# Optimization experiments

Hardware: AMD Instinct MI355X
Metric: run time of the kernel (lower is better)

Reference implementation:

```python
import jax, jax.numpy as jnp
import numpy as np

D, S, L, W, H, V = 64, 64, 64, 300, 300, 50000
NEG = jnp.float32(-9999999.0)


def setup_inputs() -> dict:
    key = jax.random.key(0)
    ks = jax.random.split(key, 16)
    n = lambda k, shape, s=0.05: jax.random.normal(k, shape, dtype=jnp.float32) * s
    return {
        "word_indices": jax.random.randint(ks[0], (D, S, L), 0, V),
        "E": n(ks[1], (V, W), 0.1),
        "W_sent": n(ks[2], (H, W)), "b_sent": jnp.zeros((H,), jnp.float32),
        "W_par": n(ks[3], (H, H)), "b_par": jnp.zeros((H,), jnp.float32),
        "W_ch": n(ks[4], (H, H)), "b_ch": jnp.zeros((H,), jnp.float32),
        "w_root": n(ks[5], (H,)), "b_root": jnp.zeros((), jnp.float32),
        "root_embed": n(ks[6], (H,)),
        "W_r": n(ks[7], (H, 3 * H)), "b_r": jnp.zeros((H,), jnp.float32),
        "W_cls": n(ks[8], (2, H)), "b_cls": jnp.zeros((2,), jnp.float32),
    }


def reference(word_indices, E, W_sent, b_sent, W_par, b_par, W_ch, b_ch,
              w_root, b_root, root_embed, W_r, b_r, W_cls, b_cls):
    lrelu = lambda x: jax.nn.leaky_relu(x, 0.01)
    # Ragged pad+gather stage of the original, dense here (all lengths == L)
    word_embed = E[word_indices]                 # [D,S,L,W]
    # 0.5*(X[l-1] + reverse(reverse(X))[l-1]) == X[l-1]; LSTM outputs unused in source
    x_last = word_embed[:, :, -1, :]             # [D,S,W]
    enc = lrelu(x_last @ W_sent.T + b_sent)      # [D,S,H] sentence encodings
    # Pairwise parent-child edge scores (O(S^2) dots in the original loops)
    P = lrelu(enc @ W_par.T + b_par)             # [D,S,H]
    C = lrelu(enc @ W_ch.T + b_ch)               # [D,S,H]
    A = jnp.einsum('dih,djh->dij', P, C)         # [D,S,S]
    A = jnp.where(jnp.eye(S, dtype=bool)[None], NEG, A)
    A = jax.nn.softmax(A, axis=1)                # Softmax(dim=0) per doc: over parents i
    scores = enc @ w_root + b_root               # [D,S] root scores
    fri = jax.nn.softmax(scores, axis=1)         # Softmax(dim=0) over sentences
    # ri[i] = r_embeds([enc_i, sum_k A[k,i]*enc_k + fri_i*root, enc_i*sum_k A[i,k]])
    tmp = jnp.einsum('dki,dkh->dih', A, enc)     # [D,S,H]
    agg = tmp + fri[..., None] * root_embed      # [D,S,H]
    tmp3 = enc * A.sum(axis=2, keepdims=True)    # [D,S,H]
    ri = lrelu(jnp.concatenate([enc, agg, tmp3], axis=-1) @ W_r.T + b_r)  # [D,S,H]
    final = ri.mean(axis=1)                      # [D,H]
    out = final @ W_cls.T + b_cls                # [D,2]
    return out, A, fri
```

## Files before the change

### kernel.cpp

```cpp
#include <hip/hip_runtime.h>

#define NEG_INF (-9999999.0f)

typedef __attribute__((ext_vector_type(8))) short bf16x8;
typedef __attribute__((ext_vector_type(4))) float f32x4;
typedef unsigned short us;
typedef unsigned int u32;

#define MFMA16 __builtin_amdgcn_mfma_f32_16x16x32_bf16

__device__ __forceinline__ float b2f(us u) {
  union { unsigned int i; float f; } x; x.i = ((unsigned int)u) << 16; return x.f;
}
__device__ __forceinline__ us f2b(float f) {
  union { float f; unsigned int i; } x; x.f = f;
  unsigned int r = x.i + 0x7fffu + ((x.i >> 16) & 1u);
  return (us)(r >> 16);
}
__device__ __forceinline__ float lrelu(float v) { return v > 0.f ? v : 0.01f * v; }
__device__ __forceinline__ bf16x8 ld8(const us* p) { return *reinterpret_cast<const bf16x8*>(p); }
__device__ __forceinline__ int swz(int row) { return (row & 7) << 4; }

__global__ __launch_bounds__(256) void k_prep0(
    const float* __restrict__ Ws, us* __restrict__ Wsb) {
  int gid = blockIdx.x * 256 + threadIdx.x;
  for (int i = gid; i < 320 * 320; i += 128 * 256) {
    int r = i / 320, c = i - r * 320;
    Wsb[i] = (r < 300 && c < 300) ? f2b(Ws[r * 300 + c]) : (us)0;
  }
}

template<int M, int NT, int KS>
__device__ __forceinline__ void sweepM(const us* __restrict__ Alds, const int (&rr)[M],
    int q, int lo, const us* __restrict__ Bg, int n0, f32x4 (&acc)[M][NT]) {
  const char* ab = (const char*)Alds;
  int ao[M], sw[M];
#pragma unroll
  for (int m = 0; m < M; ++m) { ao[m] = rr[m] * 640; sw[m] = swz(rr[m]); }
  const us* br[NT];
#pragma unroll
  for (int t = 0; t < NT; ++t)
    br[t] = Bg + (long)((n0 + t) * 16 + lo) * 320 + 8 * q;
  bf16x8 aC[M], aN[M], b0[NT], b1[NT];
#pragma unroll
  for (int m = 0; m < M; ++m) {
    aC[m] = *(const bf16x8*)(ab + ao[m] + ((16 * q) ^ sw[m]));
    aN[m] = *(const bf16x8*)(ab + ao[m] + ((64 + 16 * q) ^ sw[m]));
  }
#pragma unroll
  for (int t = 0; t < NT; ++t) b0[t] = ld8(br[t]);
#pragma unroll
  for (int t = 0; t < NT; ++t) b1[t] = ld8(br[t] + 32);
#pragma unroll
  for (int ks = 0; ks < KS - 2; ++ks) {
    bf16x8 aF[M], bF[NT];
    const int kb = 64 * (ks + 2) + 16 * q;
#pragma unroll
    for (int m = 0; m < M; ++m) aF[m] = *(const bf16x8*)(ab + ao[m] + (kb ^ sw[m]));
#pragma unroll
    for (int t = 0; t < NT; ++t) bF[t] = ld8(br[t] + (ks + 2) * 32);
#pragma unroll
    for (int t = 0; t < NT; ++t)
#pragma unroll
      for (int m = 0; m < M; ++m)
        acc[m][t] = MFMA16(aC[m], b0[t], acc[m][t], 0, 0, 0);
#pragma unroll
    for (int m = 0; m < M; ++m) { aC[m] = aN[m]; aN[m] = aF[m]; }
#pragma unroll
    for (int t = 0; t < NT; ++t) { b0[t] = b1[t]; b1[t] = bF[t]; }
  }
#pragma unroll
  for (int t = 0; t < NT; ++t)
#pragma unroll
    for (int m = 0; m < M; ++m) acc[m][t] = MFMA16(aC[m], b0[t], acc[m][t], 0, 0, 0);
#pragma unroll
  for (int t = 0; t < NT; ++t)
#pragma unroll
    for (int m = 0; m < M; ++m) acc[m][t] = MFMA16(aN[m], b1[t], acc[m][t], 0, 0, 0);
}

template<int NT, int KS>
__device__ __forceinline__ void sweepT2(const us* __restrict__ es, int q, int lo,
    const us* __restrict__ Ag, int n0, f32x4 (&acc)[2][NT]) {
  const char* eb = (const char*)es;
  int bo[2] = { lo * 640, (lo + 16) * 640 };
  int sb[2] = { swz(lo), swz(lo + 16) };
  const us* ar[NT];
#pragma unroll
  for (int t = 0; t < NT; ++t)
    ar[t] = Ag + (long)((n0 + t) * 16 + lo) * 320 + 8 * q;
  bf16x8 a0[NT], a1[NT], bC[2], bN[2];
#pragma unroll
  for (int t = 0; t < NT; ++t) a0[t] = ld8(ar[t]);
#pragma unroll
  for (int h = 0; h < 2; ++h)
    bC[h] = *(const bf16x8*)(eb + bo[h] + ((16 * q) ^ sb[h]));
#pragma unroll
  for (int t = 0; t < NT; ++t) a1[t] = ld8(ar[t] + 32);
#pragma unroll
  for (int h = 0; h < 2; ++h)
    bN[h] = *(const bf16x8*)(eb + bo[h] + ((64 + 16 * q) ^ sb[h]));
#pragma unroll
  for (int ks = 0; ks < KS - 2; ++ks) {
    bf16x8 a2[NT], bF[2];
    const int kb = 64 * (ks + 2) + 16 * q;
#pragma unroll
    for (int t = 0; t < NT; ++t) a2[t] = ld8(ar[t] + (ks + 2) * 32);
#pragma unroll
    for (int h = 0; h < 2; ++h)
      bF[h] = *(const bf16x8*)(eb + bo[h] + (kb ^ sb[h]));
#pragma unroll
    for (int t = 0; t < NT; ++t) {
      acc[0][t] = MFMA16(a0[t], bC[0], acc[0][t], 0, 0, 0);
      acc[1][t] = MFMA16(a0[t], bC[1], acc[1][t], 0, 0, 0);
    }
#pragma unroll
    for (int t = 0; t < NT; ++t) { a0[t] = a1[t]; a1[t] = a2[t]; }
#pragma unroll
    for (int h = 0; h < 2; ++h) { bC[h] = bN[h]; bN[h] = bF[h]; }
  }
#pragma unroll
  for (int t = 0; t < NT; ++t) {
    acc[0][t] = MFMA16(a0[t], bC[0], acc[0][t], 0, 0, 0);
    acc[1][t] = MFMA16(a0[t], bC[1], acc[1][t], 0, 0, 0);
  }
#pragma unroll
  for (int t = 0; t < NT; ++t) {
    acc[0][t] = MFMA16(a1[t], bN[0], acc[0][t], 0, 0, 0);
    acc[1][t] = MFMA16(a1[t], bN[1], acc[1][t], 0, 0, 0);
  }
}

template<int NT>
__device__ __forceinline__ void sweepG(const us* __restrict__ Ab,
    const us* __restrict__ Bb, int m0, int nt0, int lo, int q, int ksn, f32x4* acc) {
  const us* ar = Ab + (long)(m0 + lo) * 320 + 8 * q;
  const us* br[NT];
#pragma unroll
  for (int t = 0; t < NT; ++t)
    br[t] = Bb + (long)((nt0 + t) * 16 + lo) * 320 + 8 * q;
  bf16x8 a0 = ld8(ar), a1 = ld8(ar + 32);
  bf16x8 b0[NT], b1[NT];
#pragma unroll
  for (int t = 0; t < NT; ++t) b0[t] = ld8(br[t]);
#pragma unroll
  for (int t = 0; t < NT; ++t) b1[t] = ld8(br[t] + 32);
  for (int ks = 0; ks < ksn - 2; ++ks) {
    bf16x8 a2 = ld8(ar + (ks + 2) * 32);
    bf16x8 b2[NT];
#pragma unroll
    for (int t = 0; t < NT; ++t) b2[t] = ld8(br[t] + (ks + 2) * 32);
#pragma unroll
    for (int t = 0; t < NT; ++t)
      acc[t] = MFMA16(a0, b0[t], acc[t], 0, 0, 0);
    a0 = a1; a1 = a2;
#pragma unroll
    for (int t = 0; t < NT; ++t) { b0[t] = b1[t]; b1[t] = b2[t]; }
  }
#pragma unroll
  for (int t = 0; t < NT; ++t)
    acc[t] = MFMA16(a0, b0[t], acc[t], 0, 0, 0);
#pragma unroll
  for (int t = 0; t < NT; ++t)
    acc[t] = MFMA16(a1, b1[t], acc[t], 0, 0, 0);
}

__global__ __launch_bounds__(256) void k_encprep(
    const int* __restrict__ wi, const float* __restrict__ E,
    const us* __restrict__ Wsb, const float* __restrict__ b_sent,
    const float* __restrict__ w_root,
    const float* __restrict__ Wp, const float* __restrict__ Wc,
    const float* __restrict__ Wr, const float* __restrict__ root,
    us* __restrict__ encG, float* __restrict__ scG,
    us* __restrict__ Wpb, us* __restrict__ Wcb, us* __restrict__ Wr3b,
    float* __restrict__ c2) {
  int t = threadIdx.x;
  if (blockIdx.y == 1) {
    int gid = blockIdx.x * 256 + t;
    const int stride = 256 * 256;
    for (int i = gid; i < 5 * 102400; i += stride) {
      int p = i / 102400, rem = i - p * 102400;
      int r = rem / 320, c = rem - r * 320;
      us v = 0;
      if (r < 300 && c < 300) {
        if (p == 0)      v = f2b(Wp[r * 300 + c]);
        else if (p == 1) v = f2b(Wc[r * 300 + c]);
        else             v = f2b(Wr[r * 900 + (p - 2) * 300 + c]);
      }
      if (p == 0)      Wpb[rem] = v;
      else if (p == 1) Wcb[rem] = v;
      else             Wr3b[(p - 2) * 102400 + rem] = v;
    }
    if (gid < 2560) {
      int c = gid >> 3, p = gid & 7;
      float s = 0.f;
      if (c < 300)
        for (int h = p; h < 300; h += 8) s = fmaf(Wr[c * 900 + 300 + h], root[h], s);
      s += __shfl_xor(s, 1); s += __shfl_xor(s, 2); s += __shfl_xor(s, 4);
      if (p == 0) c2[c] = s;
    }
    return;
  }
  __shared__ __align__(16) us xs[16 * 320];
  __shared__ __align__(16) us es[16 * 320];
  int r0g = blockIdx.x * 16;
  {
    int row = t >> 4, p = t & 15;
    int widx = wi[((r0g + row) << 6) + 63];
    const float4* er = (const float4*)(E + (long)widx * 300);
    char* rowb = (char*)xs + row * 640;
    int sw = swz(row);
    for (int j = p; j < 75; j += 16) {
      float4 v = er[j];
      *(ushort4*)(rowb + ((8 * j) ^ sw)) =
          make_ushort4(f2b(v.x), f2b(v.y), f2b(v.z), f2b(v.w));
    }
    for (int c = 300 + p; c < 320; c += 16)
      *(us*)(rowb + ((2 * c) ^ sw)) = 0;
  }
  __syncthreads();
  int w = t >> 6, lane = t & 63, lo = lane & 15, q = lane >> 4;
  const f32x4 z4 = {0.f, 0.f, 0.f, 0.f};
  int rr[1] = { lo };
  f32x4 acc[1][5];
#pragma unroll
  for (int b = 0; b < 5; ++b) acc[0][b] = z4;
  sweepM<1, 5, 10>(xs, rr, q, lo, Wsb, w * 5, acc);
#pragma unroll
  for (int tt = 0; tt < 5; ++tt) {
    int col = (w * 5 + tt) * 16 + lo;
    float bb = (col < 300) ? b_sent[col] : 0.f;
#pragma unroll
    for (int r = 0; r < 4; ++r) {
      int row = 4 * q + r;
      us hv = (col < 300) ? f2b(lrelu(acc[0][tt][r] + bb)) : (us)0;
      *(us*)((char*)es + row * 640 + ((2 * col) ^ swz(row))) = hv;
      encG[(long)(r0g + row) * 320 + col] = hv;
    }
  }
  __syncthreads();
  {
    int row = t >> 4, p = t & 15;
    float s = 0.f;
    for (int cch = p; cch < 38; cch += 16) {
      bf16x8 v = *(const bf16x8*)((const char*)es + row * 640 + ((16 * cch) ^ swz(row)));
#pragma unroll
      for (int e = 0; e < 8; ++e) {
        int h = cch * 8 + e;
        if (h < 300) s = fmaf(b2f((us)v[e]), w_root[h], s);
      }
    }
    s += __shfl_xor(s, 1); s += __shfl_xor(s, 2); s += __shfl_xor(s, 4); s += __shfl_xor(s, 8);
    if (p == 0) scG[r0g + row] = s;
  }
}

__global__ __launch_bounds__(256) void k_panels(
    const us* __restrict__ encG,
    const us* __restrict__ Wpb, const us* __restrict__ Wcb, const us* __restrict__ Wrb,
    const float* __restrict__ b_par, const float* __restrict__ b_ch,
    us* __restrict__ Pg, us* __restrict__ Cg, us* __restrict__ G1g, us* __restrict__ G3g,
    us* __restrict__ G2eT) {
  __shared__ __align__(16) us es[32 * 320];
  int t = threadIdx.x, task = blockIdx.y, rt = blockIdx.x;
  {
    const float4* src = (const float4*)(encG + (long)rt * 32 * 320);
    for (int i = t; i < 1280; i += 256) {
      int row = i / 40, c16 = i - row * 40;
      float4 v = src[i];
      *(float4*)((char*)es + row * 640 + ((c16 * 16) ^ swz(row))) = v;
    }
  }
  __syncthreads();
  int w = t >> 6, lane = t & 63, lo = lane & 15, q = lane >> 4;
  const f32x4 z4 = {0.f, 0.f, 0.f, 0.f};
  if (task == 4) {
    f32x4 acc[2][5];
#pragma unroll
    for (int a = 0; a < 2; ++a)
#pragma unroll
      for (int b = 0; b < 5; ++b) acc[a][b] = z4;
    sweepT2<5, 10>(es, q, lo, Wrb + 102400, w * 5, acc);
#pragma unroll
    for (int half = 0; half < 2; ++half)
#pragma unroll
      for (int tt = 0; tt < 5; ++tt)
#pragma unroll
        for (int r = 0; r < 4; ++r) {
          int h = (w * 5 + tt) * 16 + 4 * q + r;
          G2eT[(long)h * 4096 + rt * 32 + half * 16 + lo] =
              (h < 300) ? f2b(acc[half][tt][r]) : (us)0;
        }
  } else {
    const us* Bg = (task == 0) ? Wpb : (task == 1) ? Wcb : (task == 2) ? Wrb : Wrb + 204800;
    int rr[2] = { lo, 16 + lo };
    f32x4 acc[2][5];
#pragma unroll
    for (int a = 0; a < 2; ++a)
#pragma unroll
      for (int b = 0; b < 5; ++b) acc[a][b] = z4;
    sweepM<2, 5, 10>(es, rr, q, lo, Bg, w * 5, acc);
    if (task < 2) {
      const float* bias = (task == 0) ? b_par : b_ch;
      us* outb = (task == 0) ? Pg : Cg;
#pragma unroll
      for (int m = 0; m < 2; ++m)
#pragma unroll
        for (int tt = 0; tt < 5; ++tt) {
          int col = (w * 5 + tt) * 16 + lo;
          float bb = (col < 300) ? bias[col] : 0.f;
#pragma unroll
          for (int r = 0; r < 4; ++r) {
            int row = rt * 32 + m * 16 + 4 * q + r;
            outb[(long)row * 320 + col] =
                (col < 300) ? f2b(lrelu(acc[m][tt][r] + bb)) : (us)0;
          }
        }
    } else {
      us* outb = (task == 2) ? G1g : G3g;
#pragma unroll
      for (int m = 0; m < 2; ++m)
#pragma unroll
        for (int tt = 0; tt < 5; ++tt) {
          int col = (w * 5 + tt) * 16 + lo;
          if (col < 300)
#pragma unroll
            for (int r = 0; r < 4; ++r)
              outb[(long)(rt * 32 + m * 16 + 4 * q + r) * 320 + col] = f2b(acc[m][tt][r]);
        }
    }
  }
}

__global__ __launch_bounds__(512) void k_doc(
    const us* __restrict__ Pg, const us* __restrict__ Cg, const us* __restrict__ G2eT,
    const us* __restrict__ G1g, const us* __restrict__ G3g,
    const float* __restrict__ scG, const float* __restrict__ c2,
    const float* __restrict__ b_r, const float* __restrict__ W_cls,
    const float* __restrict__ b_cls,
    float* __restrict__ outp, float* __restrict__ outA, float* __restrict__ outF) {
  __shared__ __align__(16) float LA[64 * 68];
  __shared__ __align__(16) us AtL[64 * 72];
  __shared__ float pm[512], ps[512];
  __shared__ float friS[64], rsS[64];
  __shared__ float finP2[4 * 320];
  int d = blockIdx.x, t = threadIdx.x;
  int w = t >> 6, lane = t & 63, lo = lane & 15, q = lane >> 4;
  const f32x4 z4 = {0.f, 0.f, 0.f, 0.f};

  if (t < 64) {
    float sc = scG[d * 64 + t], m = sc;
#pragma unroll
    for (int o = 32; o > 0; o >>= 1) m = fmaxf(m, __shfl_xor(m, o));
    float e = expf(sc - m), sum = e;
#pragma unroll
    for (int o = 32; o > 0; o >>= 1) sum += __shfl_xor(sum, o);
    float f = e / sum;
    friS[t] = f;
    outF[d * 64 + t] = f;
  }

  {
    const us* Pd = Pg + (long)d * 64 * 320;
    const us* Cd = Cg + (long)d * 64 * 320;
    int m = w >> 1, np = (w & 1) * 2;
    f32x4 acc2[2] = { z4, z4 };
    sweepG<2>(Pd, Cd, m * 16, np, lo, q, 10, acc2);
#pragma unroll
    for (int r = 0; r < 4; ++r) {
      int row = m * 16 + 4 * q + r;
      int c0 = np * 16 + lo, c1 = c0 + 16;
      LA[row * 68 + c0] = (row == c0) ? NEG_INF : acc2[0][r];
      LA[row * 68 + c1] = (row == c1) ? NEG_INF : acc2[1][r];
    }
  }
  __syncthreads();

  {
    int j = lane;
    float mx = -3.0e38f;
#pragma unroll
    for (int ii = 0; ii < 8; ++ii) mx = fmaxf(mx, LA[(w * 8 + ii) * 68 + j]);
    pm[w * 64 + j] = mx;
    __syncthreads();
    float gm = pm[j];
#pragma unroll
    for (int k = 1; k < 8; ++k) gm = fmaxf(gm, pm[k * 64 + j]);
    float ev[8], ss = 0.f;
#pragma unroll
    for (int ii = 0; ii < 8; ++ii) {
      float e = expf(LA[(w * 8 + ii) * 68 + j] - gm);
      ev[ii] = e; ss += e;
    }
    ps[w * 64 + j] = ss;
    __syncthreads();
    float tot = ps[j];
#pragma unroll
    for (int k = 1; k < 8; ++k) tot += ps[k * 64 + j];
    float inv = 1.f / tot;
    float* Ad = outA + (long)d * 4096;
#pragma unroll
    for (int ii = 0; ii < 8; ++ii) {
      int i = w * 8 + ii;
      float a = ev[ii] * inv;
      Ad[i * 64 + j] = a;
      AtL[j * 72 + i] = f2b(a);
      LA[i * 68 + j] = a;
    }
  }
  __syncthreads();
  if (t < 64) {
    float s = 0.f;
    for (int jj = 0; jj < 64; ++jj) s += LA[t * 68 + jj];
    rsS[t] = s;
  }
  __syncthreads();

  {
    int mg = w & 3, nh = w >> 2;
    f32x4 a10[10];
#pragma unroll
    for (int b = 0; b < 10; ++b) a10[b] = z4;
#pragma unroll
    for (int ks = 0; ks < 2; ++ks) {
      bf16x8 aA = ld8(AtL + (mg * 16 + lo) * 72 + 32 * ks + 8 * q);
#pragma unroll
      for (int tt = 0; tt < 10; ++tt) {
        bf16x8 bv = ld8(G2eT + (long)((nh * 10 + tt) * 16 + lo) * 4096 +
                        d * 64 + 32 * ks + 8 * q);
        a10[tt] = MFMA16(aA, bv, a10[tt], 0, 0, 0);
      }
    }
#pragma unroll
    for (int tt = 0; tt < 10; ++tt) {
      int col = (nh * 10 + tt) * 16 + lo;
      if (col < 300) {
        float bb = b_r[col], cc = c2[col];
        float csum = 0.f;
#pragma unroll
        for (int r = 0; r < 4; ++r) {
          int i = mg * 16 + 4 * q + r;
          float g1 = b2f(G1g[(long)(d * 64 + i) * 320 + col]);
          float g3 = b2f(G3g[(long)(d * 64 + i) * 320 + col]);
          csum += lrelu(a10[tt][r] + g1 + rsS[i] * g3 + friS[i] * cc + bb);
        }
        csum += __shfl_xor(csum, 16);
        csum += __shfl_xor(csum, 32);
        if (q == 0) finP2[mg * 320 + col] = csum;
      }
    }
  }
  __syncthreads();

  if (t < 128) {
    int cls = t >> 6, ln = t & 63;
    float s = 0.f;
    for (int h = ln; h < 300; h += 64)
      s += (finP2[h] + finP2[320 + h] + finP2[640 + h] + finP2[960 + h]) *
           W_cls[cls * 300 + h];
#pragma unroll
    for (int o = 32; o > 0; o >>= 1) s += __shfl_xor(s, o);
    if (ln == 0) outp[d * 2 + cls] = s * 0.015625f + b_cls[cls];
  }
}

extern "C" void kernel_launch(void* const* d_in, const int* in_sizes, int n_in,
                              void* d_out, int out_size, void* d_ws, size_t ws_size,
                              hipStream_t stream) {
  const int*   wi     = (const int*)d_in[0];
  const float* E      = (const float*)d_in[1];
  const float* W_sent = (const float*)d_in[2];
  const float* b_sent = (const float*)d_in[3];
  const float* W_par  = (const float*)d_in[4];
  const float* b_par  = (const float*)d_in[5];
  const float* W_ch   = (const float*)d_in[6];
  const float* b_ch   = (const float*)d_in[7];
  const float* w_root = (const float*)d_in[8];
  const float* b_root = (const float*)d_in[9];  (void)b_root;
  const float* root_e = (const float*)d_in[10];
  const float* W_r    = (const float*)d_in[11];
  const float* b_r    = (const float*)d_in[12];
  const float* W_cls  = (const float*)d_in[13];
  const float* b_cls  = (const float*)d_in[14];

  us* B = (us*)d_ws;
  us* Wsb   = B;
  us* Wpb   = B + 102400;
  us* Wcb   = B + 204800;
  us* Wr3b  = B + 307200;
  float* c2 = (float*)(B + 614400);
  us* encG  = B + 615040;
  us* Pg    = B + 1925760;
  us* Cg    = B + 3236480;
  us* G1g   = B + 4547200;
  us* G3g   = B + 5857920;
  us* G2eT  = B + 7168640;
  float* scG = (float*)(B + 8479360);

  float* outp = (float*)d_out;
  float* outA = outp + 128;
  float* outF = outp + 128 + 262144;

  k_prep0<<<128, 256, 0, stream>>>(W_sent, Wsb);
  k_encprep<<<dim3(256, 2), 256, 0, stream>>>(wi, E, Wsb, b_sent, w_root,
                                              W_par, W_ch, W_r, root_e,
                                              encG, scG, Wpb, Wcb, Wr3b, c2);
  k_panels<<<dim3(128, 5), 256, 0, stream>>>(encG, Wpb, Wcb, Wr3b,
                                             b_par, b_ch, Pg, Cg, G1g, G3g, G2eT);
  k_doc<<<64, 512, 0, stream>>>(Pg, Cg, G2eT, G1g, G3g, scG, c2,
                                b_r, W_cls, b_cls, outp, outA, outF);
}
```

Baseline: 174.1 us.

## Enlarge row tiles and store G1/G3 transposed for coalesced per-document reads

k_encprep now encodes 32 rows per block instead of 16, and its weight-conversion work moves from a second grid dimension into extra x-blocks (288 blocks in total). k_panels processes 64 rows per block, and a generalized sweepT computes G1 and G3 in transposed layout alongside G2eT. k_doc can then load four consecutive G1/G3 values per lane as one vector instead of strided scalar loads. The aim is more weight reuse per block and better-coalesced reads in the doc kernel, at the cost of fewer blocks (lower parallelism) and higher register pressure.

```diff
diff --git a/kernel.cpp b/kernel.cpp
--- a/kernel.cpp
+++ b/kernel.cpp
@@ -79,56 +79,55 @@
     for (int m = 0; m < M; ++m) acc[m][t] = MFMA16(aN[m], b1[t], acc[m][t], 0, 0, 0);
 }
 
-template<int NT, int KS>
-__device__ __forceinline__ void sweepT2(const us* __restrict__ es, int q, int lo,
-    const us* __restrict__ Ag, int n0, f32x4 (&acc)[2][NT]) {
+template<int NB, int NT, int KS>
+__device__ __forceinline__ void sweepT(const us* __restrict__ es, int q, int lo,
+    const us* __restrict__ Ag, int n0, f32x4 (&acc)[NB][NT]) {
   const char* eb = (const char*)es;
-  int bo[2] = { lo * 640, (lo + 16) * 640 };
-  int sb[2] = { swz(lo), swz(lo + 16) };
+  int bo[NB], sb[NB];
+#pragma unroll
+  for (int h = 0; h < NB; ++h) { bo[h] = (lo + 16 * h) * 640; sb[h] = swz(lo + 16 * h); }
   const us* ar[NT];
 #pragma unroll
   for (int t = 0; t < NT; ++t)
     ar[t] = Ag + (long)((n0 + t) * 16 + lo) * 320 + 8 * q;
-  bf16x8 a0[NT], a1[NT], bC[2], bN[2];
+  bf16x8 a0[NT], a1[NT], bC[NB], bN[NB];
 #pragma unroll
   for (int t = 0; t < NT; ++t) a0[t] = ld8(ar[t]);
 #pragma unroll
-  for (int h = 0; h < 2; ++h)
+  for (int h = 0; h < NB; ++h)
     bC[h] = *(const bf16x8*)(eb + bo[h] + ((16 * q) ^ sb[h]));
 #pragma unroll
   for (int t = 0; t < NT; ++t) a1[t] = ld8(ar[t] + 32);
 #pragma unroll
-  for (int h = 0; h < 2; ++h)
+  for (int h = 0; h < NB; ++h)
     bN[h] = *(const bf16x8*)(eb + bo[h] + ((64 + 16 * q) ^ sb[h]));
 #pragma unroll
   for (int ks = 0; ks < KS - 2; ++ks) {
-    bf16x8 a2[NT], bF[2];
+    bf16x8 a2[NT], bF[NB];
     const int kb = 64 * (ks + 2) + 16 * q;
 #pragma unroll
     for (int t = 0; t < NT; ++t) a2[t] = ld8(ar[t] + (ks + 2) * 32);
 #pragma unroll
-    for (int h = 0; h < 2; ++h)
+    for (int h = 0; h < NB; ++h)
       bF[h] = *(const bf16x8*)(eb + bo[h] + (kb ^ sb[h]));
 #pragma unroll
-    for (int t = 0; t < NT; ++t) {
-      acc[0][t] = MFMA16(a0[t], bC[0], acc[0][t], 0, 0, 0);
-      acc[1][t] = MFMA16(a0[t], bC[1], acc[1][t], 0, 0, 0);
-    }
+    for (int t = 0; t < NT; ++t)
+#pragma unroll
+      for (int h = 0; h < NB; ++h)
+        acc[h][t] = MFMA16(a0[t], bC[h], acc[h][t], 0, 0, 0);
 #pragma unroll
     for (int t = 0; t < NT; ++t) { a0[t] = a1[t]; a1[t] = a2[t]; }
 #pragma unroll
-    for (int h = 0; h < 2; ++h) { bC[h] = bN[h]; bN[h] = bF[h]; }
-  }
-#pragma unroll
-  for (int t = 0; t < NT; ++t) {
-    acc[0][t] = MFMA16(a0[t], bC[0], acc[0][t], 0, 0, 0);
-    acc[1][t] = MFMA16(a0[t], bC[1], acc[1][t], 0, 0, 0);
-  }
-#pragma unroll
-  for (int t = 0; t < NT; ++t) {
-    acc[0][t] = MFMA16(a1[t], bN[0], acc[0][t], 0, 0, 0);
-    acc[1][t] = MFMA16(a1[t], bN[1], acc[1][t], 0, 0, 0);
-  }
+    for (int h = 0; h < NB; ++h) { bC[h] = bN[h]; bN[h] = bF[h]; }
+  }
+#pragma unroll
+  for (int t = 0; t < NT; ++t)
+#pragma unroll
+    for (int h = 0; h < NB; ++h) acc[h][t] = MFMA16(a0[t], bC[h], acc[h][t], 0, 0, 0);
+#pragma unroll
+  for (int t = 0; t < NT; ++t)
+#pragma unroll
+    for (int h = 0; h < NB; ++h) acc[h][t] = MFMA16(a1[t], bN[h], acc[h][t], 0, 0, 0);
 }
 
 template<int NT>
@@ -175,9 +174,9 @@
     us* __restrict__ Wpb, us* __restrict__ Wcb, us* __restrict__ Wr3b,
     float* __restrict__ c2) {
   int t = threadIdx.x;
-  if (blockIdx.y == 1) {
-    int gid = blockIdx.x * 256 + t;
-    const int stride = 256 * 256;
+  if (blockIdx.x >= 128) {
+    int gid = (blockIdx.x - 128) * 256 + t;
+    const int stride = 160 * 256;
     for (int i = gid; i < 5 * 102400; i += stride) {
       int p = i / 102400, rem = i - p * 102400;
       int r = rem / 320, c = rem - r * 320;
@@ -201,48 +200,52 @@
     }
     return;
   }
-  __shared__ __align__(16) us xs[16 * 320];
-  __shared__ __align__(16) us es[16 * 320];
-  int r0g = blockIdx.x * 16;
+  __shared__ __align__(16) us xs[32 * 320];
+  __shared__ __align__(16) us es[32 * 320];
+  int r0g = blockIdx.x * 32;
   {
-    int row = t >> 4, p = t & 15;
+    int row = t >> 3, p = t & 7;
     int widx = wi[((r0g + row) << 6) + 63];
     const float4* er = (const float4*)(E + (long)widx * 300);
     char* rowb = (char*)xs + row * 640;
     int sw = swz(row);
-    for (int j = p; j < 75; j += 16) {
+    for (int j = p; j < 75; j += 8) {
       float4 v = er[j];
       *(ushort4*)(rowb + ((8 * j) ^ sw)) =
           make_ushort4(f2b(v.x), f2b(v.y), f2b(v.z), f2b(v.w));
     }
-    for (int c = 300 + p; c < 320; c += 16)
+    for (int c = 300 + p; c < 320; c += 8)
       *(us*)(rowb + ((2 * c) ^ sw)) = 0;
   }
   __syncthreads();
   int w = t >> 6, lane = t & 63, lo = lane & 15, q = lane >> 4;
   const f32x4 z4 = {0.f, 0.f, 0.f, 0.f};
-  int rr[1] = { lo };
-  f32x4 acc[1][5];
-#pragma unroll
-  for (int b = 0; b < 5; ++b) acc[0][b] = z4;
-  sweepM<1, 5, 10>(xs, rr, q, lo, Wsb, w * 5, acc);
-#pragma unroll
-  for (int tt = 0; tt < 5; ++tt) {
-    int col = (w * 5 + tt) * 16 + lo;
-    float bb = (col < 300) ? b_sent[col] : 0.f;
-#pragma unroll
-    for (int r = 0; r < 4; ++r) {
-      int row = 4 * q + r;
-      us hv = (col < 300) ? f2b(lrelu(acc[0][tt][r] + bb)) : (us)0;
-      *(us*)((char*)es + row * 640 + ((2 * col) ^ swz(row))) = hv;
-      encG[(long)(r0g + row) * 320 + col] = hv;
-    }
-  }
+  int rr[2] = { lo, 16 + lo };
+  f32x4 acc[2][5];
+#pragma unroll
+  for (int a = 0; a < 2; ++a)
+#pragma unroll
+    for (int b = 0; b < 5; ++b) acc[a][b] = z4;
+  sweepM<2, 5, 10>(xs, rr, q, lo, Wsb, w * 5, acc);
+#pragma unroll
+  for (int m = 0; m < 2; ++m)
+#pragma unroll
+    for (int tt = 0; tt < 5; ++tt) {
+      int col = (w * 5 + tt) * 16 + lo;
+      float bb = (col < 300) ? b_sent[col] : 0.f;
+#pragma unroll
+      for (int r = 0; r < 4; ++r) {
+        int row = m * 16 + 4 * q + r;
+        us hv = (col < 300) ? f2b(lrelu(acc[m][tt][r] + bb)) : (us)0;
+        *(us*)((char*)es + row * 640 + ((2 * col) ^ swz(row))) = hv;
+        encG[(long)(r0g + row) * 320 + col] = hv;
+      }
+    }
   __syncthreads();
   {
-    int row = t >> 4, p = t & 15;
+    int row = t >> 3, p = t & 7;
     float s = 0.f;
-    for (int cch = p; cch < 38; cch += 16) {
+    for (int cch = p; cch < 38; cch += 8) {
       bf16x8 v = *(const bf16x8*)((const char*)es + row * 640 + ((16 * cch) ^ swz(row)));
 #pragma unroll
       for (int e = 0; e < 8; ++e) {
@@ -250,7 +253,7 @@
         if (h < 300) s = fmaf(b2f((us)v[e]), w_root[h], s);
       }
     }
-    s += __shfl_xor(s, 1); s += __shfl_xor(s, 2); s += __shfl_xor(s, 4); s += __shfl_xor(s, 8);
+    s += __shfl_xor(s, 1); s += __shfl_xor(s, 2); s += __shfl_xor(s, 4);
     if (p == 0) scG[r0g + row] = s;
   }
 }
@@ -259,13 +262,13 @@
     const us* __restrict__ encG,
     const us* __restrict__ Wpb, const us* __restrict__ Wcb, const us* __restrict__ Wrb,
     const float* __restrict__ b_par, const float* __restrict__ b_ch,
-    us* __restrict__ Pg, us* __restrict__ Cg, us* __restrict__ G1g, us* __restrict__ G3g,
+    us* __restrict__ Pg, us* __restrict__ Cg, us* __restrict__ G1T, us* __restrict__ G3T,
     us* __restrict__ G2eT) {
-  __shared__ __align__(16) us es[32 * 320];
+  __shared__ __align__(16) us es[64 * 320];
   int t = threadIdx.x, task = blockIdx.y, rt = blockIdx.x;
   {
-    const float4* src = (const float4*)(encG + (long)rt * 32 * 320);
-    for (int i = t; i < 1280; i += 256) {
+    const float4* src = (const float4*)(encG + (long)rt * 64 * 320);
+    for (int i = t; i < 2560; i += 256) {
       int row = i / 40, c16 = i - row * 40;
       float4 v = src[i];
       *(float4*)((char*)es + row * 640 + ((c16 * 16) ^ swz(row))) = v;
@@ -274,67 +277,55 @@
   __syncthreads();
   int w = t >> 6, lane = t & 63, lo = lane & 15, q = lane >> 4;
   const f32x4 z4 = {0.f, 0.f, 0.f, 0.f};
-  if (task == 4) {
-    f32x4 acc[2][5];
-#pragma unroll
-    for (int a = 0; a < 2; ++a)
+  if (task < 2) {
+    const us* Bg = task ? Wcb : Wpb;
+    const float* bias = task ? b_ch : b_par;
+    us* outb = task ? Cg : Pg;
+    int rr[4] = { lo, 16 + lo, 32 + lo, 48 + lo };
+    f32x4 acc[4][5];
+#pragma unroll
+    for (int a = 0; a < 4; ++a)
 #pragma unroll
       for (int b = 0; b < 5; ++b) acc[a][b] = z4;
-    sweepT2<5, 10>(es, q, lo, Wrb + 102400, w * 5, acc);
-#pragma unroll
-    for (int half = 0; half < 2; ++half)
+    sweepM<4, 5, 10>(es, rr, q, lo, Bg, w * 5, acc);
+#pragma unroll
+    for (int m = 0; m < 4; ++m)
+#pragma unroll
+      for (int tt = 0; tt < 5; ++tt) {
+        int col = (w * 5 + tt) * 16 + lo;
+        float bb = (col < 300) ? bias[col] : 0.f;
+#pragma unroll
+        for (int r = 0; r < 4; ++r) {
+          int row = rt * 64 + m * 16 + 4 * q + r;
+          outb[(long)row * 320 + col] =
+              (col < 300) ? f2b(lrelu(acc[m][tt][r] + bb)) : (us)0;
+        }
+      }
+  } else {
+    const us* Ag = (task == 2) ? Wrb : (task == 3) ? Wrb + 204800 : Wrb + 102400;
+    us* outb = (task == 2) ? G1T : (task == 3) ? G3T : G2eT;
+    f32x4 acc[4][5];
+#pragma unroll
+    for (int a = 0; a < 4; ++a)
+#pragma unroll
+      for (int b = 0; b < 5; ++b) acc[a][b] = z4;
+    sweepT<4, 5, 10>(es, q, lo, Ag, w * 5, acc);
+#pragma unroll
+    for (int half = 0; half < 4; ++half)
 #pragma unroll
       for (int tt = 0; tt < 5; ++tt)
 #pragma unroll
         for (int r = 0; r < 4; ++r) {
           int h = (w * 5 + tt) * 16 + 4 * q + r;
-          G2eT[(long)h * 4096 + rt * 32 + half * 16 + lo] =
+          outb[(long)h * 4096 + rt * 64 + half * 16 + lo] =
               (h < 300) ? f2b(acc[half][tt][r]) : (us)0;
         }
-  } else {
-    const us* Bg = (task == 0) ? Wpb : (task == 1) ? Wcb : (task == 2) ? Wrb : Wrb + 204800;
-    int rr[2] = { lo, 16 + lo };
-    f32x4 acc[2][5];
-#pragma unroll
-    for (int a = 0; a < 2; ++a)
-#pragma unroll
-      for (int b = 0; b < 5; ++b) acc[a][b] = z4;
-    sweepM<2, 5, 10>(es, rr, q, lo, Bg, w * 5, acc);
-    if (task < 2) {
-      const float* bias = (task == 0) ? b_par : b_ch;
-      us* outb = (task == 0) ? Pg : Cg;
-#pragma unroll
-      for (int m = 0; m < 2; ++m)
-#pragma unroll
-        for (int tt = 0; tt < 5; ++tt) {
-          int col = (w * 5 + tt) * 16 + lo;
-          float bb = (col < 300) ? bias[col] : 0.f;
-#pragma unroll
-          for (int r = 0; r < 4; ++r) {
-            int row = rt * 32 + m * 16 + 4 * q + r;
-            outb[(long)row * 320 + col] =
-                (col < 300) ? f2b(lrelu(acc[m][tt][r] + bb)) : (us)0;
-          }
-        }
-    } else {
-      us* outb = (task == 2) ? G1g : G3g;
-#pragma unroll
-      for (int m = 0; m < 2; ++m)
-#pragma unroll
-        for (int tt = 0; tt < 5; ++tt) {
-          int col = (w * 5 + tt) * 16 + lo;
-          if (col < 300)
-#pragma unroll
-            for (int r = 0; r < 4; ++r)
-              outb[(long)(rt * 32 + m * 16 + 4 * q + r) * 320 + col] = f2b(acc[m][tt][r]);
-        }
-    }
   }
 }
 
 __global__ __launch_bounds__(512) void k_doc(
     const us* __restrict__ Pg, const us* __restrict__ Cg, const us* __restrict__ G2eT,
-    const us* __restrict__ G1g, const us* __restrict__ G3g,
+    const us* __restrict__ G1T, const us* __restrict__ G3T,
     const float* __restrict__ scG, const float* __restrict__ c2,
     const float* __restrict__ b_r, const float* __restrict__ W_cls,
     const float* __restrict__ b_cls,
@@ -436,13 +427,15 @@
       int col = (nh * 10 + tt) * 16 + lo;
       if (col < 300) {
         float bb = b_r[col], cc = c2[col];
+        ushort4 g1v = *(const ushort4*)(G1T + (long)col * 4096 + d * 64 + mg * 16 + 4 * q);
+        ushort4 g3v = *(const ushort4*)(G3T + (long)col * 4096 + d * 64 + mg * 16 + 4 * q);
+        float g1a[4] = { b2f(g1v.x), b2f(g1v.y), b2f(g1v.z), b2f(g1v.w) };
+        float g3a[4] = { b2f(g3v.x), b2f(g3v.y), b2f(g3v.z), b2f(g3v.w) };
         float csum = 0.f;
 #pragma unroll
         for (int r = 0; r < 4; ++r) {
           int i = mg * 16 + 4 * q + r;
-          float g1 = b2f(G1g[(long)(d * 64 + i) * 320 + col]);
-          float g3 = b2f(G3g[(long)(d * 64 + i) * 320 + col]);
-          csum += lrelu(a10[tt][r] + g1 + rsS[i] * g3 + friS[i] * cc + bb);
+          csum += lrelu(a10[tt][r] + g1a[r] + rsS[i] * g3a[r] + friS[i] * cc + bb);
         }
         csum += __shfl_xor(csum, 16);
         csum += __shfl_xor(csum, 32);
@@ -492,8 +485,8 @@
   us* encG  = B + 615040;
   us* Pg    = B + 1925760;
   us* Cg    = B + 3236480;
-  us* G1g   = B + 4547200;
-  us* G3g   = B + 5857920;
+  us* G1T   = B + 4547200;
+  us* G3T   = B + 5857920;
   us* G2eT  = B + 7168640;
   float* scG = (float*)(B + 8479360);
 
@@ -502,11 +495,11 @@
   float* outF = outp + 128 + 262144;
 
   k_prep0<<<128, 256, 0, stream>>>(W_sent, Wsb);
-  k_encprep<<<dim3(256, 2), 256, 0, stream>>>(wi, E, Wsb, b_sent, w_root,
-                                              W_par, W_ch, W_r, root_e,
-                                              encG, scG, Wpb, Wcb, Wr3b, c2);
-  k_panels<<<dim3(128, 5), 256, 0, stream>>>(encG, Wpb, Wcb, Wr3b,
-                                             b_par, b_ch, Pg, Cg, G1g, G3g, G2eT);
-  k_doc<<<64, 512, 0, stream>>>(Pg, Cg, G2eT, G1g, G3g, scG, c2,
+  k_encprep<<<288, 256, 0, stream>>>(wi, E, Wsb, b_sent, w_root,
+                                     W_par, W_ch, W_r, root_e,
+                                     encG, scG, Wpb, Wcb, Wr3b, c2);
+  k_panels<<<dim3(64, 5), 256, 0, stream>>>(encG, Wpb, Wcb, Wr3b,
+                                            b_par, b_ch, Pg, Cg, G1T, G3T, G2eT);
+  k_doc<<<64, 512, 0, stream>>>(Pg, Cg, G2eT, G1T, G3T, scG, c2,
                                 b_r, W_cls, b_cls, outp, outA, outF);
 }
```

Result: no change. 177.5 us (+2.0%).
